# Kernel optimization log

Measured on AMD Instinct MI355X. Metric: run time of the kernel, lower is better.

Reference implementation:

```python
import jax, jax.numpy as jnp
import numpy as np

N_NODES = 100000
N_EDGES = 625000
D_IN = 128
D_OUT = 128


def setup_inputs() -> dict:
    key = jax.random.key(0)
    k1, k2, k3, k4, k5 = jax.random.split(key, 5)
    scale = 1.0 / np.sqrt(D_IN)
    x = jax.random.normal(k1, (N_NODES, D_IN), dtype=jnp.float32)
    edge_index = jax.random.randint(k2, (2, N_EDGES), 0, N_NODES, dtype=jnp.int64)
    W_l = jax.random.normal(k3, (D_IN, D_OUT), dtype=jnp.float32) * scale
    b_l = jax.random.normal(k4, (D_OUT,), dtype=jnp.float32) * scale
    W_r = jax.random.normal(k5, (D_IN, D_OUT), dtype=jnp.float32) * scale
    return {"x": x, "edge_index": edge_index, "W_l": W_l, "b_l": b_l, "W_r": W_r}


def reference(x, edge_index, W_l, b_l, W_r):
    # SAGEConv (mean aggr, no self loops):
    #   out = lin_l(mean_{j in N(i)} x_j) + lin_r(x_i)
    src = edge_index[0]  # message source nodes
    dst = edge_index[1]  # aggregation targets
    n = x.shape[0]
    msgs = x[src]  # [E, D_IN] gather
    agg = jax.ops.segment_sum(msgs, dst, num_segments=n)  # [N, D_IN]
    deg = jax.ops.segment_sum(jnp.ones_like(dst, dtype=x.dtype), dst, num_segments=n)
    mean = agg / jnp.maximum(deg, 1.0)[:, None]  # isolated nodes -> 0
    return mean @ W_l + b_l + x @ W_r
```

## Files before the change

kernel.cpp:

```cpp
#include <hip/hip_runtime.h>


constexpr int N_NODES = 100000;
constexpr int N_EDGES = 625000;
constexpr int D = 128;
constexpr int SCAN_CHUNK = 1024;
constexpr int N_SCAN_BLOCKS = (N_NODES + SCAN_CHUNK - 1) / SCAN_CHUNK;

typedef __attribute__((ext_vector_type(8))) short short8;
typedef __attribute__((ext_vector_type(4))) short short4v;
typedef __attribute__((ext_vector_type(4))) float f32x4;

__device__ __forceinline__ unsigned short f2bf(float f) {
    union { float f; unsigned int u; } c; c.f = f;
    unsigned int u = c.u + 0x7fffu + ((c.u >> 16) & 1u);
    return (unsigned short)(u >> 16);
}
__device__ __forceinline__ float bflo(unsigned int v) {
    union { unsigned int u; float f; } c; c.u = v << 16; return c.f;
}
__device__ __forceinline__ float bfhi(unsigned int v) {
    union { unsigned int u; float f; } c; c.u = v & 0xffff0000u; return c.f;
}

__global__ __launch_bounds__(256) void csr_hist(
    const int* __restrict__ dst, int* __restrict__ cnt)
{
    int e = blockIdx.x * 256 + threadIdx.x;
    if (e < N_EDGES) atomicAdd(&cnt[dst[e]], 1);
}

__global__ __launch_bounds__(256) void scan_blocks(
    const int* __restrict__ cnt, int* __restrict__ ptr, int* __restrict__ bsums)
{
    __shared__ int sh[256];
    const int t = threadIdx.x;
    const int base = blockIdx.x * SCAN_CHUNK + t * 4;
    int v0 = (base + 0 < N_NODES) ? cnt[base + 0] : 0;
    int v1 = (base + 1 < N_NODES) ? cnt[base + 1] : 0;
    int v2 = (base + 2 < N_NODES) ? cnt[base + 2] : 0;
    int v3 = (base + 3 < N_NODES) ? cnt[base + 3] : 0;
    const int tsum = v0 + v1 + v2 + v3;
    sh[t] = tsum;
    __syncthreads();
    #pragma unroll
    for (int off = 1; off < 256; off <<= 1) {
        int val = (t >= off) ? sh[t - off] : 0;
        __syncthreads();
        sh[t] += val;
        __syncthreads();
    }
    const int texcl = sh[t] - tsum;
    if (t == 255) bsums[blockIdx.x] = sh[255];
    int e0 = texcl, e1 = e0 + v0, e2 = e1 + v1, e3 = e2 + v2;
    if (base + 0 < N_NODES) ptr[base + 0] = e0;
    if (base + 1 < N_NODES) ptr[base + 1] = e1;
    if (base + 2 < N_NODES) ptr[base + 2] = e2;
    if (base + 3 < N_NODES) ptr[base + 3] = e3;
}

__global__ __launch_bounds__(256) void add_offsets_fused(
    int* __restrict__ ptr, int* __restrict__ cursor, const int* __restrict__ bsums)
{
    __shared__ int sh[256];
    const int t = threadIdx.x;
    int v = (t < blockIdx.x) ? bsums[t] : 0;
    sh[t] = v;
    __syncthreads();
    #pragma unroll
    for (int off = 128; off > 0; off >>= 1) {
        if (t < off) sh[t] += sh[t + off];
        __syncthreads();
    }
    const int soff = sh[0];
    const int base = blockIdx.x * SCAN_CHUNK + t * 4;
    #pragma unroll
    for (int j = 0; j < 4; ++j) {
        int i = base + j;
        if (i < N_NODES) {
            int p = ptr[i] + soff;
            ptr[i] = p;
            cursor[i] = p;
        }
    }
    if (blockIdx.x == 0 && t == 0) ptr[N_NODES] = N_EDGES;
}

__global__ __launch_bounds__(256) void csr_fill(
    const int* __restrict__ src, const int* __restrict__ dst,
    int* __restrict__ cursor, int* __restrict__ sorted_src)
{
    int e = blockIdx.x * 256 + threadIdx.x;
    if (e < N_EDGES) {
        int t = dst[e];
        int pos = atomicAdd(&cursor[t], 1);
        sorted_src[pos] = src[e];
    }
}

__global__ __launch_bounds__(256) void prep_bf(
    const float* __restrict__ x, const float* __restrict__ Wl,
    const float* __restrict__ Wr,
    unsigned short* __restrict__ xb, unsigned short* __restrict__ wT)
{
    const int XC = N_NODES * D / 8;
    int c = blockIdx.x * 256 + threadIdx.x;
    if (c < XC) {
        const float4* xp = (const float4*)x;
        float4 a = xp[(size_t)c * 2];
        float4 b = xp[(size_t)c * 2 + 1];
        short8 v;
        v[0] = (short)f2bf(a.x); v[1] = (short)f2bf(a.y);
        v[2] = (short)f2bf(a.z); v[3] = (short)f2bf(a.w);
        v[4] = (short)f2bf(b.x); v[5] = (short)f2bf(b.y);
        v[6] = (short)f2bf(b.z); v[7] = (short)f2bf(b.w);
        ((short8*)xb)[c] = v;
    } else if (c < XC + 4096) {
        int idx = c - XC;
        int n  = idx >> 5;
        int k0 = (idx & 31) * 8;
        short8 v;
        #pragma unroll
        for (int j = 0; j < 8; ++j) {
            int k = k0 + j;
            float f = (k < 128) ? Wl[k * 128 + n] : Wr[(k - 128) * 128 + n];
            v[j] = (short)f2bf(f);
        }
        *(short8*)&wT[n * 256 + k0] = v;
    }
}

__global__ __launch_bounds__(256) void wt_build(
    const float* __restrict__ Wl, const float* __restrict__ Wr,
    unsigned short* __restrict__ wT)
{
    int idx = blockIdx.x * 256 + threadIdx.x;
    if (idx >= 128 * 256) return;
    int n = idx >> 8;
    int k = idx & 255;
    float v = (k < 128) ? Wl[k * 128 + n] : Wr[(k - 128) * 128 + n];
    wT[n * 256 + k] = f2bf(v);
}

template<bool MBF>
__global__ __launch_bounds__(256) void sage_aggregate_bf(
    const unsigned short* __restrict__ xb,
    const int* __restrict__ ptr,
    const int* __restrict__ sorted_src,
    unsigned short* __restrict__ mean_bf,
    float* __restrict__ mean_f32)
{
    const int node = blockIdx.x * 16 + (threadIdx.x >> 4);
    if (node >= N_NODES) return;
    const int l = threadIdx.x & 15;
    const int beg = ptr[node];
    const int end = ptr[node + 1];
    const size_t off = (size_t)l * 8;

    float a0=0,a1=0,a2=0,a3=0,a4=0,a5=0,a6=0,a7=0;
    float b0=0,b1=0,b2=0,b3=0,b4=0,b5=0,b6=0,b7=0;
    float c0=0,c1=0,c2=0,c3=0,c4=0,c5=0,c6=0,c7=0;
    float d0=0,d1=0,d2=0,d3=0,d4=0,d5=0,d6=0,d7=0;

    int i = beg;
    for (; i + 3 < end; i += 4) {
        int s0 = sorted_src[i],     s1 = sorted_src[i + 1];
        int s2 = sorted_src[i + 2], s3 = sorted_src[i + 3];
        uint4 v0 = *(const uint4*)&xb[(size_t)s0 * D + off];
        uint4 v1 = *(const uint4*)&xb[(size_t)s1 * D + off];
        uint4 v2 = *(const uint4*)&xb[(size_t)s2 * D + off];
        uint4 v3 = *(const uint4*)&xb[(size_t)s3 * D + off];
        a0+=bflo(v0.x); a1+=bfhi(v0.x); a2+=bflo(v0.y); a3+=bfhi(v0.y);
        a4+=bflo(v0.z); a5+=bfhi(v0.z); a6+=bflo(v0.w); a7+=bfhi(v0.w);
        b0+=bflo(v1.x); b1+=bfhi(v1.x); b2+=bflo(v1.y); b3+=bfhi(v1.y);
        b4+=bflo(v1.z); b5+=bfhi(v1.z); b6+=bflo(v1.w); b7+=bfhi(v1.w);
        c0+=bflo(v2.x); c1+=bfhi(v2.x); c2+=bflo(v2.y); c3+=bfhi(v2.y);
        c4+=bflo(v2.z); c5+=bfhi(v2.z); c6+=bflo(v2.w); c7+=bfhi(v2.w);
        d0+=bflo(v3.x); d1+=bfhi(v3.x); d2+=bflo(v3.y); d3+=bfhi(v3.y);
        d4+=bflo(v3.z); d5+=bfhi(v3.z); d6+=bflo(v3.w); d7+=bfhi(v3.w);
    }
    for (; i < end; ++i) {
        int s0 = sorted_src[i];
        uint4 v0 = *(const uint4*)&xb[(size_t)s0 * D + off];
        a0+=bflo(v0.x); a1+=bfhi(v0.x); a2+=bflo(v0.y); a3+=bfhi(v0.y);
        a4+=bflo(v0.z); a5+=bfhi(v0.z); a6+=bflo(v0.w); a7+=bfhi(v0.w);
    }
    const float sc = 1.0f / fmaxf((float)(end - beg), 1.0f);
    float r0 = ((a0+b0)+(c0+d0))*sc, r1 = ((a1+b1)+(c1+d1))*sc;
    float r2 = ((a2+b2)+(c2+d2))*sc, r3 = ((a3+b3)+(c3+d3))*sc;
    float r4 = ((a4+b4)+(c4+d4))*sc, r5 = ((a5+b5)+(c5+d5))*sc;
    float r6 = ((a6+b6)+(c6+d6))*sc, r7 = ((a7+b7)+(c7+d7))*sc;

    if constexpr (MBF) {
        uint4 o;
        o.x = (unsigned)f2bf(r0) | ((unsigned)f2bf(r1) << 16);
        o.y = (unsigned)f2bf(r2) | ((unsigned)f2bf(r3) << 16);
        o.z = (unsigned)f2bf(r4) | ((unsigned)f2bf(r5) << 16);
        o.w = (unsigned)f2bf(r6) | ((unsigned)f2bf(r7) << 16);
        *(uint4*)&mean_bf[(size_t)node * D + off] = o;
    } else {
        *(float4*)&mean_f32[(size_t)node * D + off] = make_float4(r0, r1, r2, r3);
        *(float4*)&mean_f32[(size_t)node * D + off + 4] = make_float4(r4, r5, r6, r7);
    }
}

template<bool MBF>
__global__ __launch_bounds__(256) void sage_gemm_bf(
    const unsigned short* __restrict__ xb,
    const unsigned short* __restrict__ mean_bf,
    const unsigned short* __restrict__ wT,
    const float* __restrict__ bl,
    float* __restrict__ out)
{
    __shared__ unsigned short sW[128 * 256];
    __shared__ unsigned short sA[32 * 256];

    const int tid  = threadIdx.x;
    const int lane = tid & 63;
    const int w    = tid >> 6;
    const int l15  = lane & 15;
    const int lg   = lane >> 4;

    #pragma unroll
    for (int i = 0; i < 16; ++i) {
        int c  = tid + i * 256;
        int n  = c >> 5;
        int k8 = c & 31;
        short8 v = ((const short8*)wT)[c];
        *(short8*)&sW[n * 256 + ((k8 ^ (n & 7)) << 3)] = v;
    }

    const int a_r0 = l15;
    const int a_r1 = 16 + l15;
    const int n0 = w * 32 + l15;
    const int n1 = n0 + 16;
    const float bias0 = bl[n0];
    const float bias1 = bl[n1];

    const int nTiles = N_NODES / 32;

    for (int tile = blockIdx.x; tile < nTiles; tile += gridDim.x) {
        const int row0 = tile * 32;

        if constexpr (MBF) {
            #pragma unroll
            for (int i = 0; i < 4; ++i) {
                int c = tid + i * 256;
                int r = c >> 5;
                int s = c & 31;
                const unsigned short* srcp = (s < 16)
                    ? &mean_bf[(size_t)(row0 + r) * D + s * 8]
                    : &xb[(size_t)(row0 + r) * D + (s - 16) * 8];
                short8 v = *(const short8*)srcp;
                *(short8*)&sA[r * 256 + ((s ^ (r & 7)) << 3)] = v;
            }
        } else {
            #pragma unroll
            for (int i = 0; i < 4; ++i) {
                int c = tid + i * 256;
                int r = c >> 5;
                int f4 = c & 31;
                float4 v = *(const float4*)&out[(size_t)(row0 + r) * D + f4 * 4];
                short4v b;
                b.x = (short)f2bf(v.x); b.y = (short)f2bf(v.y);
                b.z = (short)f2bf(v.z); b.w = (short)f2bf(v.w);
                int u = f4 >> 1;
                *(short4v*)&sA[r * 256 + ((u ^ (r & 7)) << 3) + (f4 & 1) * 4] = b;
            }
            #pragma unroll
            for (int i = 0; i < 2; ++i) {
                int c = tid + i * 256;
                int r = c >> 4;
                int s = 16 + (c & 15);
                short8 v = *(const short8*)&xb[(size_t)(row0 + r) * D + (c & 15) * 8];
                *(short8*)&sA[r * 256 + ((s ^ (r & 7)) << 3)] = v;
            }
        }
        __syncthreads();

        f32x4 acc00 = {0.f,0.f,0.f,0.f}, acc01 = {0.f,0.f,0.f,0.f};
        f32x4 acc10 = {0.f,0.f,0.f,0.f}, acc11 = {0.f,0.f,0.f,0.f};

        #pragma unroll
        for (int s = 0; s < 8; ++s) {
            int ks = s * 4 + lg;
            short8 a0 = *(const short8*)&sA[a_r0 * 256 + ((ks ^ (a_r0 & 7)) << 3)];
            short8 a1 = *(const short8*)&sA[a_r1 * 256 + ((ks ^ (a_r1 & 7)) << 3)];
            short8 b0 = *(const short8*)&sW[n0 * 256 + ((ks ^ (n0 & 7)) << 3)];
            short8 b1 = *(const short8*)&sW[n1 * 256 + ((ks ^ (n1 & 7)) << 3)];
            acc00 = __builtin_amdgcn_mfma_f32_16x16x32_bf16(a0, b0, acc00, 0, 0, 0);
            acc01 = __builtin_amdgcn_mfma_f32_16x16x32_bf16(a0, b1, acc01, 0, 0, 0);
            acc10 = __builtin_amdgcn_mfma_f32_16x16x32_bf16(a1, b0, acc10, 0, 0, 0);
            acc11 = __builtin_amdgcn_mfma_f32_16x16x32_bf16(a1, b1, acc11, 0, 0, 0);
        }
        __syncthreads();

        #pragma unroll
        for (int reg = 0; reg < 4; ++reg) {
            int r0w = row0 + lg * 4 + reg;
            int r1w = r0w + 16;
            out[(size_t)r0w * D + n0] = acc00[reg] + bias0;
            out[(size_t)r0w * D + n1] = acc01[reg] + bias1;
            out[(size_t)r1w * D + n0] = acc10[reg] + bias0;
            out[(size_t)r1w * D + n1] = acc11[reg] + bias1;
        }
    }
}

__global__ __launch_bounds__(256) void sage_aggregate(
    const float* __restrict__ x,
    const int* __restrict__ ptr,
    const int* __restrict__ sorted_src,
    float* __restrict__ mean)
{
    const int node = blockIdx.x * 4 + (threadIdx.x >> 6);
    if (node >= N_NODES) return;
    const int lane = threadIdx.x & 63;
    const int beg = ptr[node];
    const int end = ptr[node + 1];

    float2 acc0 = make_float2(0.f, 0.f);
    float2 acc1 = make_float2(0.f, 0.f);
    int i = beg;
    for (; i + 1 < end; i += 2) {
        int s0 = sorted_src[i];
        int s1 = sorted_src[i + 1];
        float2 a = *(const float2*)&x[(size_t)s0 * D + lane * 2];
        float2 b = *(const float2*)&x[(size_t)s1 * D + lane * 2];
        acc0.x += a.x; acc0.y += a.y;
        acc1.x += b.x; acc1.y += b.y;
    }
    if (i < end) {
        int s0 = sorted_src[i];
        float2 a = *(const float2*)&x[(size_t)s0 * D + lane * 2];
        acc0.x += a.x; acc0.y += a.y;
    }
    const float sc = 1.0f / fmaxf((float)(end - beg), 1.0f);
    float2 r = make_float2((acc0.x + acc1.x) * sc, (acc0.y + acc1.y) * sc);
    *(float2*)&mean[(size_t)node * D + lane * 2] = r;
}

__global__ __launch_bounds__(256) void sage_gemm_mfma(
    const float* __restrict__ x,
    const unsigned short* __restrict__ wT,
    const float* __restrict__ bl,
    float* __restrict__ out)
{
    __shared__ unsigned short sW[128 * 256];
    __shared__ unsigned short sA[32 * 256];

    const int tid  = threadIdx.x;
    const int lane = tid & 63;
    const int w    = tid >> 6;
    const int l15  = lane & 15;
    const int lg   = lane >> 4;

    #pragma unroll
    for (int i = 0; i < 16; ++i) {
        int c  = tid + i * 256;
        int n  = c >> 5;
        int k8 = c & 31;
        short8 v = ((const short8*)wT)[c];
        *(short8*)&sW[n * 256 + ((k8 ^ (n & 7)) << 3)] = v;
    }

    const int a_r0 = l15;
    const int a_r1 = 16 + l15;
    const int n0 = w * 32 + l15;
    const int n1 = n0 + 16;
    const float bias0 = bl[n0];
    const float bias1 = bl[n1];
    const int nTiles = N_NODES / 32;

    for (int tile = blockIdx.x; tile < nTiles; tile += gridDim.x) {
        const int row0 = tile * 32;
        #pragma unroll
        for (int i = 0; i < 8; ++i) {
            int c    = tid + i * 256;
            int r    = c >> 6;
            int half = (c >> 5) & 1;
            int f4   = c & 31;
            const float* srcp = half ? &x[(size_t)(row0 + r) * D + f4 * 4]
                                     : &out[(size_t)(row0 + r) * D + f4 * 4];
            float4 v = *(const float4*)srcp;
            short4v b;
            b.x = (short)f2bf(v.x); b.y = (short)f2bf(v.y);
            b.z = (short)f2bf(v.z); b.w = (short)f2bf(v.w);
            int k = half * 128 + f4 * 4;
            int u = k >> 3;
            *(short4v*)&sA[r * 256 + ((u ^ (r & 7)) << 3) + (k & 7)] = b;
        }
        __syncthreads();

        f32x4 acc00 = {0.f,0.f,0.f,0.f}, acc01 = {0.f,0.f,0.f,0.f};
        f32x4 acc10 = {0.f,0.f,0.f,0.f}, acc11 = {0.f,0.f,0.f,0.f};

        #pragma unroll
        for (int s = 0; s < 8; ++s) {
            int ks = s * 4 + lg;
            short8 a0 = *(const short8*)&sA[a_r0 * 256 + ((ks ^ (a_r0 & 7)) << 3)];
            short8 a1 = *(const short8*)&sA[a_r1 * 256 + ((ks ^ (a_r1 & 7)) << 3)];
            short8 b0 = *(const short8*)&sW[n0 * 256 + ((ks ^ (n0 & 7)) << 3)];
            short8 b1 = *(const short8*)&sW[n1 * 256 + ((ks ^ (n1 & 7)) << 3)];
            acc00 = __builtin_amdgcn_mfma_f32_16x16x32_bf16(a0, b0, acc00, 0, 0, 0);
            acc01 = __builtin_amdgcn_mfma_f32_16x16x32_bf16(a0, b1, acc01, 0, 0, 0);
            acc10 = __builtin_amdgcn_mfma_f32_16x16x32_bf16(a1, b0, acc10, 0, 0, 0);
            acc11 = __builtin_amdgcn_mfma_f32_16x16x32_bf16(a1, b1, acc11, 0, 0, 0);
        }
        __syncthreads();

        #pragma unroll
        for (int reg = 0; reg < 4; ++reg) {
            int r0w = row0 + lg * 4 + reg;
            int r1w = r0w + 16;
            out[(size_t)r0w * D + n0] = acc00[reg] + bias0;
            out[(size_t)r0w * D + n1] = acc01[reg] + bias1;
            out[(size_t)r1w * D + n0] = acc10[reg] + bias0;
            out[(size_t)r1w * D + n1] = acc11[reg] + bias1;
        }
    }
}

__global__ __launch_bounds__(256) void sage_scatter(
    const float* __restrict__ x, const int* __restrict__ src,
    const int* __restrict__ dst, float* __restrict__ agg, float* __restrict__ deg)
{
    int gid = blockIdx.x * 256 + threadIdx.x;
    int e = gid >> 7;
    if (e >= N_EDGES) return;
    int d = gid & 127;
    atomicAdd(&agg[(size_t)dst[e] * D + d], x[(size_t)src[e] * D + d]);
    if (d == 0) atomicAdd(&deg[dst[e]], 1.0f);
}

__global__ __launch_bounds__(256) void apply_mean(
    float* __restrict__ agg, const float* __restrict__ deg)
{
    int gid = blockIdx.x * 256 + threadIdx.x;
    int row = gid >> 5;
    if (row >= N_NODES) return;
    float sc = 1.0f / fmaxf(deg[row], 1.0f);
    float4 v = ((float4*)agg)[gid];
    v.x *= sc; v.y *= sc; v.z *= sc; v.w *= sc;
    ((float4*)agg)[gid] = v;
}

__device__ __forceinline__ void accum_tile(
    float acc[4][4], const float (*sWf)[D], const float (*srow)[D], int h, int j4)
{
    #pragma unroll 2
    for (int k = 0; k < D; k += 4) {
        float4 w0 = *(const float4*)&sWf[k + 0][j4];
        float4 w1 = *(const float4*)&sWf[k + 1][j4];
        float4 w2 = *(const float4*)&sWf[k + 2][j4];
        float4 w3 = *(const float4*)&sWf[k + 3][j4];
        #pragma unroll
        for (int r = 0; r < 4; ++r) {
            float4 a = *(const float4*)&srow[h + r * 8][k];
            acc[r][0] = fmaf(a.x, w0.x, fmaf(a.y, w1.x, fmaf(a.z, w2.x, fmaf(a.w, w3.x, acc[r][0]))));
            acc[r][1] = fmaf(a.x, w0.y, fmaf(a.y, w1.y, fmaf(a.z, w2.y, fmaf(a.w, w3.y, acc[r][1]))));
            acc[r][2] = fmaf(a.x, w0.z, fmaf(a.y, w1.z, fmaf(a.z, w2.z, fmaf(a.w, w3.z, acc[r][2]))));
            acc[r][3] = fmaf(a.x, w0.w, fmaf(a.y, w1.w, fmaf(a.z, w2.w, fmaf(a.w, w3.w, acc[r][3]))));
        }
    }
}

__global__ __launch_bounds__(256) void sage_gemm_f32(
    const float* __restrict__ x, const float* __restrict__ Wl,
    const float* __restrict__ bl, const float* __restrict__ Wr,
    float* __restrict__ out)
{
    __shared__ float sWf[D][D];
    __shared__ float srow[32][D];
    const int tid = threadIdx.x;
    const int j4 = (tid & 31) * 4;
    const int h  = tid >> 5;
    const int nTiles = (N_NODES + 31) / 32;
    const float4 bias = *(const float4*)(bl + j4);

    for (int tile = blockIdx.x; tile < nTiles; tile += gridDim.x) {
        const int row0 = tile * 32;
        float acc[4][4];
        #pragma unroll
        for (int r = 0; r < 4; ++r)
            #pragma unroll
            for (int c = 0; c < 4; ++c) acc[r][c] = 0.0f;

        __syncthreads();
        #pragma unroll
        for (int i = 0; i < 16; ++i)
            ((float4*)sWf)[tid + i * 256] = ((const float4*)Wl)[tid + i * 256];
        #pragma unroll
        for (int i = 0; i < 4; ++i) {
            int idx = tid + i * 256, r = idx >> 5, c = idx & 31, row = row0 + r;
            float4 v = make_float4(0.f,0.f,0.f,0.f);
            if (row < N_NODES) v = ((const float4*)out)[(size_t)row * 32 + c];
            ((float4*)srow)[idx] = v;
        }
        __syncthreads();
        accum_tile(acc, sWf, srow, h, j4);

        __syncthreads();
        #pragma unroll
        for (int i = 0; i < 16; ++i)
            ((float4*)sWf)[tid + i * 256] = ((const float4*)Wr)[tid + i * 256];
        #pragma unroll
        for (int i = 0; i < 4; ++i) {
            int idx = tid + i * 256, r = idx >> 5, c = idx & 31, row = row0 + r;
            float4 v = make_float4(0.f,0.f,0.f,0.f);
            if (row < N_NODES) v = ((const float4*)x)[(size_t)row * 32 + c];
            ((float4*)srow)[idx] = v;
        }
        __syncthreads();
        accum_tile(acc, sWf, srow, h, j4);

        #pragma unroll
        for (int r = 0; r < 4; ++r) {
            int row = row0 + h + r * 8;
            if (row < N_NODES) {
                float4 v = make_float4(acc[r][0] + bias.x, acc[r][1] + bias.y,
                                       acc[r][2] + bias.z, acc[r][3] + bias.w);
                *(float4*)(out + (size_t)row * D + j4) = v;
            }
        }
    }
}

extern "C" void kernel_launch(void* const* d_in, const int* in_sizes, int n_in,
                              void* d_out, int out_size, void* d_ws, size_t ws_size,
                              hipStream_t stream) {
    const float* x   = (const float*)d_in[0];
    const int*   ei  = (const int*)d_in[1];
    const float* Wl  = (const float*)d_in[2];
    const float* bl  = (const float*)d_in[3];
    const float* Wr  = (const float*)d_in[4];
    float* out = (float*)d_out;

    const int* src = ei;
    const int* dst = ei + N_EDGES;

    int* cnt    = (int*)d_ws;
    int* ptr    = cnt + N_NODES;
    int* cursor = ptr + N_NODES + 1;
    int* bsums  = cursor + N_NODES;
    int* sorted = bsums + 128;
    unsigned short* wT      = (unsigned short*)(sorted + N_EDGES);
    unsigned short* xb      = wT + 128 * 256;
    unsigned short* mean_bf = xb + (size_t)N_NODES * D;

    size_t base_ints = (size_t)(3 * N_NODES + 1 + 128 + N_EDGES);
    size_t need_B  = base_ints * sizeof(int);
    size_t need_A2 = need_B + 128 * 256 * 2 + (size_t)N_NODES * D * 2;
    size_t need_A  = need_A2 + (size_t)N_NODES * D * 2;

    if (ws_size >= need_B) {
        hipMemsetAsync(cnt, 0, (size_t)N_NODES * sizeof(int), stream);
        csr_hist<<<(N_EDGES + 255) / 256, 256, 0, stream>>>(dst, cnt);
        scan_blocks<<<N_SCAN_BLOCKS, 256, 0, stream>>>(cnt, ptr, bsums);
        add_offsets_fused<<<N_SCAN_BLOCKS, 256, 0, stream>>>(ptr, cursor, bsums);
        csr_fill<<<(N_EDGES + 255) / 256, 256, 0, stream>>>(src, dst, cursor, sorted);

        if (ws_size >= need_A) {
            prep_bf<<<(N_NODES * D / 8 + 4096 + 255) / 256, 256, 0, stream>>>(x, Wl, Wr, xb, wT);
            sage_aggregate_bf<true><<<(N_NODES + 15) / 16, 256, 0, stream>>>(
                xb, ptr, sorted, mean_bf, nullptr);
            sage_gemm_bf<true><<<512, 256, 0, stream>>>(xb, mean_bf, wT, bl, out);
        } else if (ws_size >= need_A2) {
            prep_bf<<<(N_NODES * D / 8 + 4096 + 255) / 256, 256, 0, stream>>>(x, Wl, Wr, xb, wT);
            sage_aggregate_bf<false><<<(N_NODES + 15) / 16, 256, 0, stream>>>(
                xb, ptr, sorted, nullptr, out);
            sage_gemm_bf<false><<<512, 256, 0, stream>>>(xb, nullptr, wT, bl, out);
        } else {
            unsigned short* wTc = (unsigned short*)cursor;
            wt_build<<<(128 * 256 + 255) / 256, 256, 0, stream>>>(Wl, Wr, wTc);
            sage_aggregate<<<(N_NODES + 3) / 4, 256, 0, stream>>>(x, ptr, sorted, out);
            sage_gemm_mfma<<<512, 256, 0, stream>>>(x, wTc, bl, out);
        }
    } else {
        float* deg = (float*)d_ws;
        hipMemsetAsync(out, 0, (size_t)N_NODES * D * sizeof(float), stream);
        hipMemsetAsync(deg, 0, (size_t)N_NODES * sizeof(float), stream);
        long long total = (long long)N_EDGES * 128;
        sage_scatter<<<(int)((total + 255) / 256), 256, 0, stream>>>(x, src, dst, out, deg);
        apply_mean<<<(N_NODES * 32 + 255) / 256, 256, 0, stream>>>(out, deg);
        sage_gemm_f32<<<512, 256, 0, stream>>>(x, Wl, bl, Wr, out);
    }
}
```

Baseline: 144.9 us.

## Fuse histogram into bf16 prep, predicate aggregate tail, keep weights in registers

The edge-degree histogram moves into the x/weight bf16 conversion kernel, which removes one launch and lets the atomics overlap with the conversion traffic. The aggregate loop replaces its scalar remainder loop with a predicated 4-wide step that clamps indices and zero-weights the invalid lanes, so tail edges keep full memory-level parallelism at the cost of redundant loads. The GEMM now holds B fragments in registers instead of staging a 64KB weight tile in LDS, which raises occupancy, and the grid grows to 768 blocks. The fallback paths are simplified and the workspace offset is aligned.

Result: faster. 138.2 us (-4.6%).

```diff
diff --git a/kernel.cpp b/kernel.cpp
--- a/kernel.cpp
+++ b/kernel.cpp
@@ -23,85 +23,11 @@
     union { unsigned int u; float f; } c; c.u = v & 0xffff0000u; return c.f;
 }
 
-__global__ __launch_bounds__(256) void csr_hist(
-    const int* __restrict__ dst, int* __restrict__ cnt)
-{
-    int e = blockIdx.x * 256 + threadIdx.x;
-    if (e < N_EDGES) atomicAdd(&cnt[dst[e]], 1);
-}
-
-__global__ __launch_bounds__(256) void scan_blocks(
-    const int* __restrict__ cnt, int* __restrict__ ptr, int* __restrict__ bsums)
-{
-    __shared__ int sh[256];
-    const int t = threadIdx.x;
-    const int base = blockIdx.x * SCAN_CHUNK + t * 4;
-    int v0 = (base + 0 < N_NODES) ? cnt[base + 0] : 0;
-    int v1 = (base + 1 < N_NODES) ? cnt[base + 1] : 0;
-    int v2 = (base + 2 < N_NODES) ? cnt[base + 2] : 0;
-    int v3 = (base + 3 < N_NODES) ? cnt[base + 3] : 0;
-    const int tsum = v0 + v1 + v2 + v3;
-    sh[t] = tsum;
-    __syncthreads();
-    #pragma unroll
-    for (int off = 1; off < 256; off <<= 1) {
-        int val = (t >= off) ? sh[t - off] : 0;
-        __syncthreads();
-        sh[t] += val;
-        __syncthreads();
-    }
-    const int texcl = sh[t] - tsum;
-    if (t == 255) bsums[blockIdx.x] = sh[255];
-    int e0 = texcl, e1 = e0 + v0, e2 = e1 + v1, e3 = e2 + v2;
-    if (base + 0 < N_NODES) ptr[base + 0] = e0;
-    if (base + 1 < N_NODES) ptr[base + 1] = e1;
-    if (base + 2 < N_NODES) ptr[base + 2] = e2;
-    if (base + 3 < N_NODES) ptr[base + 3] = e3;
-}
-
-__global__ __launch_bounds__(256) void add_offsets_fused(
-    int* __restrict__ ptr, int* __restrict__ cursor, const int* __restrict__ bsums)
-{
-    __shared__ int sh[256];
-    const int t = threadIdx.x;
-    int v = (t < blockIdx.x) ? bsums[t] : 0;
-    sh[t] = v;
-    __syncthreads();
-    #pragma unroll
-    for (int off = 128; off > 0; off >>= 1) {
-        if (t < off) sh[t] += sh[t + off];
-        __syncthreads();
-    }
-    const int soff = sh[0];
-    const int base = blockIdx.x * SCAN_CHUNK + t * 4;
-    #pragma unroll
-    for (int j = 0; j < 4; ++j) {
-        int i = base + j;
-        if (i < N_NODES) {
-            int p = ptr[i] + soff;
-            ptr[i] = p;
-            cursor[i] = p;
-        }
-    }
-    if (blockIdx.x == 0 && t == 0) ptr[N_NODES] = N_EDGES;
-}
-
-__global__ __launch_bounds__(256) void csr_fill(
-    const int* __restrict__ src, const int* __restrict__ dst,
-    int* __restrict__ cursor, int* __restrict__ sorted_src)
-{
-    int e = blockIdx.x * 256 + threadIdx.x;
-    if (e < N_EDGES) {
-        int t = dst[e];
-        int pos = atomicAdd(&cursor[t], 1);
-        sorted_src[pos] = src[e];
-    }
-}
-
-__global__ __launch_bounds__(256) void prep_bf(
+__global__ __launch_bounds__(256) void prep_hist(
     const float* __restrict__ x, const float* __restrict__ Wl,
-    const float* __restrict__ Wr,
-    unsigned short* __restrict__ xb, unsigned short* __restrict__ wT)
+    const float* __restrict__ Wr, const int* __restrict__ dst,
+    unsigned short* __restrict__ xb, unsigned short* __restrict__ wT,
+    int* __restrict__ cnt)
 {
     const int XC = N_NODES * D / 8;
     int c = blockIdx.x * 256 + threadIdx.x;
@@ -127,19 +53,85 @@
             v[j] = (short)f2bf(f);
         }
         *(short8*)&wT[n * 256 + k0] = v;
-    }
-}
-
-__global__ __launch_bounds__(256) void wt_build(
-    const float* __restrict__ Wl, const float* __restrict__ Wr,
-    unsigned short* __restrict__ wT)
-{
-    int idx = blockIdx.x * 256 + threadIdx.x;
-    if (idx >= 128 * 256) return;
-    int n = idx >> 8;
-    int k = idx & 255;
-    float v = (k < 128) ? Wl[k * 128 + n] : Wr[(k - 128) * 128 + n];
-    wT[n * 256 + k] = f2bf(v);
+    } else if (c < XC + 4096 + N_EDGES) {
+        int e = c - XC - 4096;
+        atomicAdd(&cnt[dst[e]], 1);
+    }
+}
+
+__global__ __launch_bounds__(256) void csr_hist(
+    const int* __restrict__ dst, int* __restrict__ cnt)
+{
+    int e = blockIdx.x * 256 + threadIdx.x;
+    if (e < N_EDGES) atomicAdd(&cnt[dst[e]], 1);
+}
+
+__global__ __launch_bounds__(256) void scan_blocks(
+    const int* __restrict__ cnt, int* __restrict__ ptr, int* __restrict__ bsums)
+{
+    __shared__ int sh[256];
+    const int t = threadIdx.x;
+    const int base = blockIdx.x * SCAN_CHUNK + t * 4;
+    int v0 = (base + 0 < N_NODES) ? cnt[base + 0] : 0;
+    int v1 = (base + 1 < N_NODES) ? cnt[base + 1] : 0;
+    int v2 = (base + 2 < N_NODES) ? cnt[base + 2] : 0;
+    int v3 = (base + 3 < N_NODES) ? cnt[base + 3] : 0;
+    const int tsum = v0 + v1 + v2 + v3;
+    sh[t] = tsum;
+    __syncthreads();
+    #pragma unroll
+    for (int off = 1; off < 256; off <<= 1) {
+        int val = (t >= off) ? sh[t - off] : 0;
+        __syncthreads();
+        sh[t] += val;
+        __syncthreads();
+    }
+    const int texcl = sh[t] - tsum;
+    if (t == 255) bsums[blockIdx.x] = sh[255];
+    int e0 = texcl, e1 = e0 + v0, e2 = e1 + v1, e3 = e2 + v2;
+    if (base + 0 < N_NODES) ptr[base + 0] = e0;
+    if (base + 1 < N_NODES) ptr[base + 1] = e1;
+    if (base + 2 < N_NODES) ptr[base + 2] = e2;
+    if (base + 3 < N_NODES) ptr[base + 3] = e3;
+}
+
+__global__ __launch_bounds__(256) void add_offsets_fused(
+    int* __restrict__ ptr, int* __restrict__ cursor, const int* __restrict__ bsums)
+{
+    __shared__ int sh[256];
+    const int t = threadIdx.x;
+    int v = (t < blockIdx.x) ? bsums[t] : 0;
+    sh[t] = v;
+    __syncthreads();
+    #pragma unroll
+    for (int off = 128; off > 0; off >>= 1) {
+        if (t < off) sh[t] += sh[t + off];
+        __syncthreads();
+    }
+    const int soff = sh[0];
+    const int base = blockIdx.x * SCAN_CHUNK + t * 4;
+    #pragma unroll
+    for (int j = 0; j < 4; ++j) {
+        int i = base + j;
+        if (i < N_NODES) {
+            int p = ptr[i] + soff;
+            ptr[i] = p;
+            cursor[i] = p;
+        }
+    }
+    if (blockIdx.x == 0 && t == 0) ptr[N_NODES] = N_EDGES;
+}
+
+__global__ __launch_bounds__(256) void csr_fill(
+    const int* __restrict__ src, const int* __restrict__ dst,
+    int* __restrict__ cursor, int* __restrict__ sorted_src)
+{
+    int e = blockIdx.x * 256 + threadIdx.x;
+    if (e < N_EDGES) {
+        int t = dst[e];
+        int pos = atomicAdd(&cursor[t], 1);
+        sorted_src[pos] = src[e];
+    }
 }
 
 template<bool MBF>
@@ -162,28 +154,34 @@
     float c0=0,c1=0,c2=0,c3=0,c4=0,c5=0,c6=0,c7=0;
     float d0=0,d1=0,d2=0,d3=0,d4=0,d5=0,d6=0,d7=0;
 
-    int i = beg;
-    for (; i + 3 < end; i += 4) {
-        int s0 = sorted_src[i],     s1 = sorted_src[i + 1];
-        int s2 = sorted_src[i + 2], s3 = sorted_src[i + 3];
+    for (int i = beg; i < end; i += 4) {
+        int last = end - 1;
+        int e1 = i + 1 < end ? i + 1 : last;
+        int e2 = i + 2 < end ? i + 2 : last;
+        int e3 = i + 3 < end ? i + 3 : last;
+        float w1 = (i + 1 < end) ? 1.f : 0.f;
+        float w2 = (i + 2 < end) ? 1.f : 0.f;
+        float w3 = (i + 3 < end) ? 1.f : 0.f;
+        int s0 = sorted_src[i],  s1 = sorted_src[e1];
+        int s2 = sorted_src[e2], s3 = sorted_src[e3];
         uint4 v0 = *(const uint4*)&xb[(size_t)s0 * D + off];
         uint4 v1 = *(const uint4*)&xb[(size_t)s1 * D + off];
         uint4 v2 = *(const uint4*)&xb[(size_t)s2 * D + off];
         uint4 v3 = *(const uint4*)&xb[(size_t)s3 * D + off];
         a0+=bflo(v0.x); a1+=bfhi(v0.x); a2+=bflo(v0.y); a3+=bfhi(v0.y);
         a4+=bflo(v0.z); a5+=bfhi(v0.z); a6+=bflo(v0.w); a7+=bfhi(v0.w);
-        b0+=bflo(v1.x); b1+=bfhi(v1.x); b2+=bflo(v1.y); b3+=bfhi(v1.y);
-        b4+=bflo(v1.z); b5+=bfhi(v1.z); b6+=bflo(v1.w); b7+=bfhi(v1.w);
-        c0+=bflo(v2.x); c1+=bfhi(v2.x); c2+=bflo(v2.y); c3+=bfhi(v2.y);
-        c4+=bflo(v2.z); c5+=bfhi(v2.z); c6+=bflo(v2.w); c7+=bfhi(v2.w);
-        d0+=bflo(v3.x); d1+=bfhi(v3.x); d2+=bflo(v3.y); d3+=bfhi(v3.y);
-        d4+=bflo(v3.z); d5+=bfhi(v3.z); d6+=bflo(v3.w); d7+=bfhi(v3.w);
-    }
-    for (; i < end; ++i) {
-        int s0 = sorted_src[i];
-        uint4 v0 = *(const uint4*)&xb[(size_t)s0 * D + off];
-        a0+=bflo(v0.x); a1+=bfhi(v0.x); a2+=bflo(v0.y); a3+=bfhi(v0.y);
-        a4+=bflo(v0.z); a5+=bfhi(v0.z); a6+=bflo(v0.w); a7+=bfhi(v0.w);
+        b0=fmaf(w1,bflo(v1.x),b0); b1=fmaf(w1,bfhi(v1.x),b1);
+        b2=fmaf(w1,bflo(v1.y),b2); b3=fmaf(w1,bfhi(v1.y),b3);
+        b4=fmaf(w1,bflo(v1.z),b4); b5=fmaf(w1,bfhi(v1.z),b5);
+        b6=fmaf(w1,bflo(v1.w),b6); b7=fmaf(w1,bfhi(v1.w),b7);
+        c0=fmaf(w2,bflo(v2.x),c0); c1=fmaf(w2,bfhi(v2.x),c1);
+        c2=fmaf(w2,bflo(v2.y),c2); c3=fmaf(w2,bfhi(v2.y),c3);
+        c4=fmaf(w2,bflo(v2.z),c4); c5=fmaf(w2,bfhi(v2.z),c5);
+        c6=fmaf(w2,bflo(v2.w),c6); c7=fmaf(w2,bfhi(v2.w),c7);
+        d0=fmaf(w3,bflo(v3.x),d0); d1=fmaf(w3,bfhi(v3.x),d1);
+        d2=fmaf(w3,bflo(v3.y),d2); d3=fmaf(w3,bfhi(v3.y),d3);
+        d4=fmaf(w3,bflo(v3.z),d4); d5=fmaf(w3,bfhi(v3.z),d5);
+        d6=fmaf(w3,bflo(v3.w),d6); d7=fmaf(w3,bfhi(v3.w),d7);
     }
     const float sc = 1.0f / fmaxf((float)(end - beg), 1.0f);
     float r0 = ((a0+b0)+(c0+d0))*sc, r1 = ((a1+b1)+(c1+d1))*sc;
@@ -204,15 +202,13 @@
     }
 }
 
-template<bool MBF>
-__global__ __launch_bounds__(256) void sage_gemm_bf(
+__global__ __launch_bounds__(256) void sage_gemm_rb(
     const unsigned short* __restrict__ xb,
     const unsigned short* __restrict__ mean_bf,
     const unsigned short* __restrict__ wT,
     const float* __restrict__ bl,
     float* __restrict__ out)
 {
-    __shared__ unsigned short sW[128 * 256];
     __shared__ unsigned short sA[32 * 256];
 
     const int tid  = threadIdx.x;
@@ -221,19 +217,18 @@
     const int l15  = lane & 15;
     const int lg   = lane >> 4;
 
+    const int n0 = w * 32 + l15;
+    const int n1 = n0 + 16;
+
+    short8 B0[8], B1[8];
     #pragma unroll
-    for (int i = 0; i < 16; ++i) {
-        int c  = tid + i * 256;
-        int n  = c >> 5;
-        int k8 = c & 31;
-        short8 v = ((const short8*)wT)[c];
-        *(short8*)&sW[n * 256 + ((k8 ^ (n & 7)) << 3)] = v;
+    for (int s = 0; s < 8; ++s) {
+        B0[s] = *(const short8*)&wT[(size_t)n0 * 256 + s * 32 + lg * 8];
+        B1[s] = *(const short8*)&wT[(size_t)n1 * 256 + s * 32 + lg * 8];
     }
 
     const int a_r0 = l15;
     const int a_r1 = 16 + l15;
-    const int n0 = w * 32 + l15;
-    const int n1 = n0 + 16;
     const float bias0 = bl[n0];
     const float bias1 = bl[n1];
 
@@ -242,39 +237,16 @@
     for (int tile = blockIdx.x; tile < nTiles; tile += gridDim.x) {
         const int row0 = tile * 32;
 
-        if constexpr (MBF) {
-            #pragma unroll
-            for (int i = 0; i < 4; ++i) {
-                int c = tid + i * 256;
-                int r = c >> 5;
-                int s = c & 31;
-                const unsigned short* srcp = (s < 16)
-                    ? &mean_bf[(size_t)(row0 + r) * D + s * 8]
-                    : &xb[(size_t)(row0 + r) * D + (s - 16) * 8];
-                short8 v = *(const short8*)srcp;
-                *(short8*)&sA[r * 256 + ((s ^ (r & 7)) << 3)] = v;
-            }
-        } else {
-            #pragma unroll
-            for (int i = 0; i < 4; ++i) {
-                int c = tid + i * 256;
-                int r = c >> 5;
-                int f4 = c & 31;
-                float4 v = *(const float4*)&out[(size_t)(row0 + r) * D + f4 * 4];
-                short4v b;
-                b.x = (short)f2bf(v.x); b.y = (short)f2bf(v.y);
-                b.z = (short)f2bf(v.z); b.w = (short)f2bf(v.w);
-                int u = f4 >> 1;
-                *(short4v*)&sA[r * 256 + ((u ^ (r & 7)) << 3) + (f4 & 1) * 4] = b;
-            }
-            #pragma unroll
-            for (int i = 0; i < 2; ++i) {
-                int c = tid + i * 256;
-                int r = c >> 4;
-                int s = 16 + (c & 15);
-                short8 v = *(const short8*)&xb[(size_t)(row0 + r) * D + (c & 15) * 8];
-                *(short8*)&sA[r * 256 + ((s ^ (r & 7)) << 3)] = v;
-            }
+        #pragma unroll
+        for (int i = 0; i < 4; ++i) {
+            int c = tid + i * 256;
+            int r = c >> 5;
+            int s = c & 31;
+            const unsigned short* srcp = (s < 16)
+                ? &mean_bf[(size_t)(row0 + r) * D + s * 8]
+                : &xb[(size_t)(row0 + r) * D + (s - 16) * 8];
+            short8 v = *(const short8*)srcp;
+            *(short8*)&sA[r * 256 + ((s ^ (r & 7)) << 3)] = v;
         }
         __syncthreads();
 
@@ -286,12 +258,10 @@
             int ks = s * 4 + lg;
             short8 a0 = *(const short8*)&sA[a_r0 * 256 + ((ks ^ (a_r0 & 7)) << 3)];
             short8 a1 = *(const short8*)&sA[a_r1 * 256 + ((ks ^ (a_r1 & 7)) << 3)];
-            short8 b0 = *(const short8*)&sW[n0 * 256 + ((ks ^ (n0 & 7)) << 3)];
-            short8 b1 = *(const short8*)&sW[n1 * 256 + ((ks ^ (n1 & 7)) << 3)];
-            acc00 = __builtin_amdgcn_mfma_f32_16x16x32_bf16(a0, b0, acc00, 0, 0, 0);
-            acc01 = __builtin_amdgcn_mfma_f32_16x16x32_bf16(a0, b1, acc01, 0, 0, 0);
-            acc10 = __builtin_amdgcn_mfma_f32_16x16x32_bf16(a1, b0, acc10, 0, 0, 0);
-            acc11 = __builtin_amdgcn_mfma_f32_16x16x32_bf16(a1, b1, acc11, 0, 0, 0);
+            acc00 = __builtin_amdgcn_mfma_f32_16x16x32_bf16(a0, B0[s], acc00, 0, 0, 0);
+            acc01 = __builtin_amdgcn_mfma_f32_16x16x32_bf16(a0, B1[s], acc01, 0, 0, 0);
+            acc10 = __builtin_amdgcn_mfma_f32_16x16x32_bf16(a1, B0[s], acc10, 0, 0, 0);
+            acc11 = __builtin_amdgcn_mfma_f32_16x16x32_bf16(a1, B1[s], acc11, 0, 0, 0);
         }
         __syncthreads();
 
@@ -305,6 +275,18 @@
             out[(size_t)r1w * D + n1] = acc11[reg] + bias1;
         }
     }
+}
+
+__global__ __launch_bounds__(256) void wt_build(
+    const float* __restrict__ Wl, const float* __restrict__ Wr,
+    unsigned short* __restrict__ wT)
+{
+    int idx = blockIdx.x * 256 + threadIdx.x;
+    if (idx >= 128 * 256) return;
+    int n = idx >> 8;
+    int k = idx & 255;
+    float v = (k < 128) ? Wl[k * 128 + n] : Wr[(k - 128) * 128 + n];
+    wT[n * 256 + k] = f2bf(v);
 }
 
 __global__ __launch_bounds__(256) void sage_aggregate(
@@ -544,38 +526,36 @@
     int* cursor = ptr + N_NODES + 1;
     int* bsums  = cursor + N_NODES;
     int* sorted = bsums + 128;
-    unsigned short* wT      = (unsigned short*)(sorted + N_EDGES);
+    size_t int_count = (size_t)(3 * N_NODES + 1 + 128 + N_EDGES);
+    int_count = (int_count + 7) & ~(size_t)7;
+    unsigned short* wT      = (unsigned short*)((int*)d_ws + int_count);
     unsigned short* xb      = wT + 128 * 256;
     unsigned short* mean_bf = xb + (size_t)N_NODES * D;
 
-    size_t base_ints = (size_t)(3 * N_NODES + 1 + 128 + N_EDGES);
-    size_t need_B  = base_ints * sizeof(int);
-    size_t need_A2 = need_B + 128 * 256 * 2 + (size_t)N_NODES * D * 2;
-    size_t need_A  = need_A2 + (size_t)N_NODES * D * 2;
-
-    if (ws_size >= need_B) {
+    size_t need_B  = int_count * sizeof(int);
+    size_t need_A  = need_B + 128 * 256 * 2 + 2 * (size_t)N_NODES * D * 2;
+
+    if (ws_size >= need_A) {
+        hipMemsetAsync(cnt, 0, (size_t)N_NODES * sizeof(int), stream);
+        const int PREP_TOTAL = N_NODES * D / 8 + 4096 + N_EDGES;
+        prep_hist<<<(PREP_TOTAL + 255) / 256, 256, 0, stream>>>(
+            x, Wl, Wr, dst, xb, wT, cnt);
+        scan_blocks<<<N_SCAN_BLOCKS, 256, 0, stream>>>(cnt, ptr, bsums);
+        add_offsets_fused<<<N_SCAN_BLOCKS, 256, 0, stream>>>(ptr, cursor, bsums);
+        csr_fill<<<(N_EDGES + 255) / 256, 256, 0, stream>>>(src, dst, cursor, sorted);
+        sage_aggregate_bf<true><<<(N_NODES + 15) / 16, 256, 0, stream>>>(
+            xb, ptr, sorted, mean_bf, nullptr);
+        sage_gemm_rb<<<768, 256, 0, stream>>>(xb, mean_bf, wT, bl, out);
+    } else if (ws_size >= need_B) {
         hipMemsetAsync(cnt, 0, (size_t)N_NODES * sizeof(int), stream);
         csr_hist<<<(N_EDGES + 255) / 256, 256, 0, stream>>>(dst, cnt);
         scan_blocks<<<N_SCAN_BLOCKS, 256, 0, stream>>>(cnt, ptr, bsums);
         add_offsets_fused<<<N_SCAN_BLOCKS, 256, 0, stream>>>(ptr, cursor, bsums);
         csr_fill<<<(N_EDGES + 255) / 256, 256, 0, stream>>>(src, dst, cursor, sorted);
-
-        if (ws_size >= need_A) {
-            prep_bf<<<(N_NODES * D / 8 + 4096 + 255) / 256, 256, 0, stream>>>(x, Wl, Wr, xb, wT);
-            sage_aggregate_bf<true><<<(N_NODES + 15) / 16, 256, 0, stream>>>(
-                xb, ptr, sorted, mean_bf, nullptr);
-            sage_gemm_bf<true><<<512, 256, 0, stream>>>(xb, mean_bf, wT, bl, out);
-        } else if (ws_size >= need_A2) {
-            prep_bf<<<(N_NODES * D / 8 + 4096 + 255) / 256, 256, 0, stream>>>(x, Wl, Wr, xb, wT);
-            sage_aggregate_bf<false><<<(N_NODES + 15) / 16, 256, 0, stream>>>(
-                xb, ptr, sorted, nullptr, out);
-            sage_gemm_bf<false><<<512, 256, 0, stream>>>(xb, nullptr, wT, bl, out);
-        } else {
-            unsigned short* wTc = (unsigned short*)cursor;
-            wt_build<<<(128 * 256 + 255) / 256, 256, 0, stream>>>(Wl, Wr, wTc);
-            sage_aggregate<<<(N_NODES + 3) / 4, 256, 0, stream>>>(x, ptr, sorted, out);
-            sage_gemm_mfma<<<512, 256, 0, stream>>>(x, wTc, bl, out);
-        }
+        unsigned short* wTc = (unsigned short*)cursor;
+        wt_build<<<(128 * 256 + 255) / 256, 256, 0, stream>>>(Wl, Wr, wTc);
+        sage_aggregate<<<(N_NODES + 3) / 4, 256, 0, stream>>>(x, ptr, sorted, out);
+        sage_gemm_mfma<<<512, 256, 0, stream>>>(x, wTc, bl, out);
     } else {
         float* deg = (float*)d_ws;
         hipMemsetAsync(out, 0, (size_t)N_NODES * D * sizeof(float), stream);
```
